# Optimization experiments

Hardware: AMD Instinct MI355X
Metric: run time of the kernel (lower is better)

Reference implementation:

```python
import jax, jax.numpy as jnp
import numpy as np

N = 100000      # total sampled nodes
NT = 20000      # target (destination) nodes
E = 2000000     # edges
IN = 128        # in_dim
OUT = 64        # out_channels (heads=1, concat)
NEG_SLOPE = 0.2 # GATConv default negative_slope


def setup_inputs() -> dict:
    key = jax.random.key(0)
    ks = jax.random.split(key, 6)
    x = jax.random.normal(ks[0], (N, IN), dtype=jnp.float32)
    edge_src = jax.random.randint(ks[1], (E,), 0, N)
    edge_dst = jax.random.randint(ks[2], (E,), 0, NT)
    # GATConv params: shared lin for src/dst (in_channels is int), att vectors, bias
    W = jax.random.normal(ks[3], (IN, OUT), dtype=jnp.float32) / np.sqrt(IN).astype(np.float32)
    att_src = jax.random.normal(ks[4], (OUT,), dtype=jnp.float32)
    att_dst = jax.random.normal(ks[5], (OUT,), dtype=jnp.float32)
    bias = jnp.zeros((OUT,), dtype=jnp.float32)
    return {"x": x, "edge_src": edge_src, "edge_dst": edge_dst,
            "W": W, "att_src": att_src, "att_dst": att_dst, "bias": bias,
            "num_target": NT}


def reference(x, edge_src, edge_dst, W, att_src, att_dst, bias, num_target):
    # Linear transform (lin_src == lin_dst in PyG GATConv when in_channels is int)
    x_proj = x @ W                      # [N, OUT]
    x_dst = x_proj[:num_target]         # [NT, OUT] target nodes are x[:num_target]
    # Per-node attention logits
    a_src = x_proj @ att_src            # [N]
    a_dst = x_dst @ att_dst             # [NT]
    # Edge logits + LeakyReLU
    e = jax.nn.leaky_relu(a_src[edge_src] + a_dst[edge_dst], NEG_SLOPE)  # [E]
    # Segment softmax over edges grouped by destination
    m = jax.ops.segment_max(e, edge_dst, num_segments=num_target)
    m = jnp.where(jnp.isneginf(m), jnp.float32(0.0), m)  # empty segments
    p = jnp.exp(e - m[edge_dst])
    denom = jax.ops.segment_sum(p, edge_dst, num_segments=num_target)
    alpha = p / (denom[edge_dst] + jnp.float32(1e-16))   # PyG softmax eps
    # Weighted scatter-aggregate of source features
    out = jax.ops.segment_sum(alpha[:, None] * x_proj[edge_src], edge_dst,
                              num_segments=num_target)   # [NT, OUT]
    return out + bias
```

## Files before the change

kernel.cpp:

```cpp
#include <hip/hip_runtime.h>

#define IN_DIM 128
#define OUT_DIM 64
#define NEG_SLOPE 0.2f

#define NBUCK 625
#define BCAP 4096
#define CHUNK 8192

typedef __attribute__((ext_vector_type(8))) short short8v;
typedef __attribute__((ext_vector_type(4))) float f32x4;

__device__ __forceinline__ unsigned pack_bf16(float a, float b) {
    unsigned ua = __float_as_uint(a), ub = __float_as_uint(b);
    ua += 0x7FFFu + ((ua >> 16) & 1u);
    ub += 0x7FFFu + ((ub >> 16) & 1u);
    return (ua >> 16) | (ub & 0xFFFF0000u);
}

__device__ __forceinline__ short8v mk8(unsigned a, unsigned b, unsigned c, unsigned d) {
    union { uint4 u; short8v s; } z;
    z.u = make_uint4(a, b, c, d);
    return z.s;
}

__global__ __launch_bounds__(1024) void part_kernel(
    const float* __restrict__ W, unsigned* __restrict__ w_hi,
    unsigned* __restrict__ w_lo,
    const int* __restrict__ edge_src, const int* __restrict__ edge_dst,
    int* __restrict__ bcursor, unsigned* __restrict__ inter, int E)
{
    if (blockIdx.x == 0) {
        int g = threadIdx.x;
        int kb = g >> 6, col = g & 63;
        unsigned uh[4], ul[4];
#pragma unroll
        for (int i = 0; i < 4; ++i) {
            float a = W[(kb * 8 + 2 * i) * 64 + col];
            float b = W[(kb * 8 + 2 * i + 1) * 64 + col];
            unsigned h = pack_bf16(a, b);
            float la = a - __uint_as_float(h << 16);
            float lb = b - __uint_as_float(h & 0xFFFF0000u);
            uh[i] = h;
            ul[i] = pack_bf16(la, lb);
        }
        *(uint4*)(w_hi + g * 4) = make_uint4(uh[0], uh[1], uh[2], uh[3]);
        *(uint4*)(w_lo + g * 4) = make_uint4(ul[0], ul[1], ul[2], ul[3]);
        return;
    }

    __shared__ unsigned stage[CHUNK];
    __shared__ int hist[NBUCK];
    __shared__ int loff[NBUCK];
    __shared__ int gbase[NBUCK];
    __shared__ int cur[NBUCK];
    __shared__ int wsum[16];

    const int t  = threadIdx.x;
    const int c0 = (blockIdx.x - 1) * CHUNK;
    const int cnt = min(CHUNK, E - c0);

    for (int i = t; i < NBUCK; i += 1024) hist[i] = 0;
    __syncthreads();

    unsigned pk[8];
    int nmine = 0;
    const int i0 = 8 * t;
    if (i0 + 8 <= cnt) {
        int4 s0 = *(const int4*)(edge_src + c0 + i0);
        int4 s1 = *(const int4*)(edge_src + c0 + i0 + 4);
        int4 d0 = *(const int4*)(edge_dst + c0 + i0);
        int4 d1 = *(const int4*)(edge_dst + c0 + i0 + 4);
        pk[0] = ((unsigned)d0.x << 17) | (unsigned)s0.x;
        pk[1] = ((unsigned)d0.y << 17) | (unsigned)s0.y;
        pk[2] = ((unsigned)d0.z << 17) | (unsigned)s0.z;
        pk[3] = ((unsigned)d0.w << 17) | (unsigned)s0.w;
        pk[4] = ((unsigned)d1.x << 17) | (unsigned)s1.x;
        pk[5] = ((unsigned)d1.y << 17) | (unsigned)s1.y;
        pk[6] = ((unsigned)d1.z << 17) | (unsigned)s1.z;
        pk[7] = ((unsigned)d1.w << 17) | (unsigned)s1.w;
        nmine = 8;
    } else {
#pragma unroll
        for (int k = 0; k < 8; ++k) {
            int i = i0 + k;
            if (i < cnt) {
                pk[k] = ((unsigned)edge_dst[c0 + i] << 17) | (unsigned)edge_src[c0 + i];
                nmine = k + 1;
            }
        }
    }
#pragma unroll
    for (int k = 0; k < 8; ++k)
        if (k < nmine) atomicAdd(&hist[pk[k] >> 22], 1);
    __syncthreads();

    {
        const int lane = t & 63, w = t >> 6;
        int v = (t < NBUCK) ? hist[t] : 0;
        int scan = v;
#pragma unroll
        for (int off = 1; off < 64; off <<= 1) {
            int o = __shfl_up(scan, off);
            if (lane >= off) scan += o;
        }
        if (lane == 63) wsum[w] = scan;
        __syncthreads();
        int wpre = 0;
#pragma unroll
        for (int i = 0; i < 16; ++i)
            if (i < w) wpre += wsum[i];
        int excl = wpre + scan - v;
        if (t < NBUCK) {
            loff[t] = excl;
            cur[t]  = excl;
            if (v > 0) gbase[t] = t * BCAP + atomicAdd(&bcursor[t], v);
        }
    }
    __syncthreads();

#pragma unroll
    for (int k = 0; k < 8; ++k)
        if (k < nmine) {
            unsigned v = pk[k];
            int p = atomicAdd(&cur[v >> 22], 1);
            stage[p] = v;
        }
    __syncthreads();

    for (int i = t; i < cnt; i += 1024) {
        unsigned v = stage[i];
        int b = v >> 22;
        int pos = gbase[b] + (i - loff[b]);
        if (pos < (b + 1) * BCAP) inter[pos] = v;
    }
}

__global__ __launch_bounds__(256) void gemm_kernel(
    const float* __restrict__ x,
    const unsigned* __restrict__ w_hi, const unsigned* __restrict__ w_lo,
    const float* __restrict__ att_src, const float* __restrict__ att_dst,
    unsigned* __restrict__ x_bf, float* __restrict__ a_src,
    float* __restrict__ a_dst, int N, int NT)
{
    __shared__ __align__(16) float C[128 * 64];

    const int t    = threadIdx.x;
    const int lane = t & 63;
    const int w    = t >> 6;
    const int r0   = blockIdx.x * 128;
    const int rsub = lane & 15;
    const int kg   = lane >> 4;

    const int r1 = min(r0 + 32 * w + rsub,      N - 1);
    const int r2 = min(r0 + 32 * w + 16 + rsub, N - 1);
    const float* xrow1 = x + (size_t)r1 * IN_DIM + kg * 8;
    const float* xrow2 = x + (size_t)r2 * IN_DIM + kg * 8;

    float4 xv[16];
#pragma unroll
    for (int j = 0; j < 8; ++j)
        xv[j] = *(const float4*)(xrow1 + (j >> 1) * 32 + (j & 1) * 4);
#pragma unroll
    for (int j = 0; j < 8; ++j)
        xv[8 + j] = *(const float4*)(xrow2 + (j >> 1) * 32 + (j & 1) * 4);
    __builtin_amdgcn_sched_barrier(0);

    short8v ah[2][4], al[2][4];
#pragma unroll
    for (int rf = 0; rf < 2; ++rf)
#pragma unroll
        for (int ks = 0; ks < 4; ++ks) {
            float4 v0 = xv[8 * rf + 2 * ks], v1 = xv[8 * rf + 2 * ks + 1];
            unsigned h0 = pack_bf16(v0.x, v0.y);
            unsigned h1 = pack_bf16(v0.z, v0.w);
            unsigned h2 = pack_bf16(v1.x, v1.y);
            unsigned h3 = pack_bf16(v1.z, v1.w);
            unsigned l0 = pack_bf16(v0.x - __uint_as_float(h0 << 16),
                                    v0.y - __uint_as_float(h0 & 0xFFFF0000u));
            unsigned l1 = pack_bf16(v0.z - __uint_as_float(h1 << 16),
                                    v0.w - __uint_as_float(h1 & 0xFFFF0000u));
            unsigned l2 = pack_bf16(v1.x - __uint_as_float(h2 << 16),
                                    v1.y - __uint_as_float(h2 & 0xFFFF0000u));
            unsigned l3 = pack_bf16(v1.z - __uint_as_float(h3 << 16),
                                    v1.w - __uint_as_float(h3 & 0xFFFF0000u));
            ah[rf][ks] = mk8(h0, h1, h2, h3);
            al[rf][ks] = mk8(l0, l1, l2, l3);
        }

    f32x4 acc[2][4];
#pragma unroll
    for (int rf = 0; rf < 2; ++rf)
#pragma unroll
        for (int cf = 0; cf < 4; ++cf) acc[rf][cf] = f32x4{0.f, 0.f, 0.f, 0.f};

#pragma unroll
    for (int ks = 0; ks < 4; ++ks) {
        const int kb = 4 * ks + kg;
        const unsigned* bhp = w_hi + (kb * 64 + rsub) * 4;
        const unsigned* blp = w_lo + (kb * 64 + rsub) * 4;
        short8v bh[4], bl[4];
#pragma unroll
        for (int cf = 0; cf < 4; ++cf) {
            bh[cf] = *(const short8v*)(bhp + cf * 64);
            bl[cf] = *(const short8v*)(blp + cf * 64);
        }
#pragma unroll
        for (int cf = 0; cf < 4; ++cf) {
#pragma unroll
            for (int rf = 0; rf < 2; ++rf) {
                acc[rf][cf] = __builtin_amdgcn_mfma_f32_16x16x32_bf16(ah[rf][ks], bh[cf], acc[rf][cf], 0, 0, 0);
                acc[rf][cf] = __builtin_amdgcn_mfma_f32_16x16x32_bf16(al[rf][ks], bh[cf], acc[rf][cf], 0, 0, 0);
                acc[rf][cf] = __builtin_amdgcn_mfma_f32_16x16x32_bf16(ah[rf][ks], bl[cf], acc[rf][cf], 0, 0, 0);
            }
        }
    }

#pragma unroll
    for (int rf = 0; rf < 2; ++rf)
#pragma unroll
        for (int cf = 0; cf < 4; ++cf)
#pragma unroll
            for (int j = 0; j < 4; ++j) {
                int row = 32 * w + 16 * rf + 4 * kg + j;
                int col = 16 * cf + rsub;
                C[row * 64 + ((col + 4 * row) & 63)] = acc[rf][cf][j];
            }
    __syncthreads();

    {
        const int row = t >> 1;
        const int h   = t & 1;
        const int rr  = r0 + row;
        float v[32];
#pragma unroll
        for (int j = 0; j < 8; ++j) {
            int s = (32 * h + 4 * j + 4 * row) & 63;
            float4 f = *(const float4*)(C + row * 64 + s);
            v[4 * j + 0] = f.x; v[4 * j + 1] = f.y;
            v[4 * j + 2] = f.z; v[4 * j + 3] = f.w;
        }
        if (rr < N) {
            unsigned pk[16];
#pragma unroll
            for (int m = 0; m < 16; ++m)
                pk[m] = pack_bf16(v[2 * m], v[2 * m + 1]);
            unsigned* dst = x_bf + (size_t)rr * 32 + h * 16;
            *(uint4*)(dst + 0)  = make_uint4(pk[0], pk[1], pk[2], pk[3]);
            *(uint4*)(dst + 4)  = make_uint4(pk[4], pk[5], pk[6], pk[7]);
            *(uint4*)(dst + 8)  = make_uint4(pk[8], pk[9], pk[10], pk[11]);
            *(uint4*)(dst + 12) = make_uint4(pk[12], pk[13], pk[14], pk[15]);

            float ps = 0.f, pd = 0.f;
#pragma unroll
            for (int i = 0; i < 32; ++i) {
                ps = fmaf(v[i], att_src[32 * h + i], ps);
                pd = fmaf(v[i], att_dst[32 * h + i], pd);
            }
            ps += __shfl_xor(ps, 1);
            pd += __shfl_xor(pd, 1);
            if (h == 0) {
                a_src[rr] = ps;
                if (rr < NT) a_dst[rr] = pd;
            }
        }
    }
}

#define LRELU_EXP(a) __expf(((a) > 0.f ? (a) : NEG_SLOPE * (a)))

__global__ __launch_bounds__(512) void agg_kernel(
    const int* __restrict__ bcursor, const unsigned* __restrict__ inter,
    const float* __restrict__ a_src, const float* __restrict__ a_dst,
    const unsigned* __restrict__ x_bf, const float* __restrict__ bias,
    float* __restrict__ out, int NT)
{
    __shared__ unsigned ssrc[BCAP];
    __shared__ int cnt[32], off_[32], cur[32];

    const int b = blockIdx.x;
    const int t = threadIdx.x;
    const int base = b * BCAP;
    const int n = min(bcursor[b], BCAP);

    if (t < 32) cnt[t] = 0;
    __syncthreads();

    unsigned ev[8];
#pragma unroll
    for (int k = 0; k < 8; ++k) {
        int i = t + 512 * k;
        ev[k] = 0xFFFFFFFFu;
        if (i < n) {
            ev[k] = inter[base + i];
            atomicAdd(&cnt[(ev[k] >> 17) & 31], 1);
        }
    }
    __syncthreads();

    if (t == 0) {
        int r = 0;
#pragma unroll
        for (int j = 0; j < 32; ++j) { off_[j] = r; r += cnt[j]; }
    }
    __syncthreads();
    if (t < 32) cur[t] = off_[t];
    __syncthreads();

#pragma unroll
    for (int k = 0; k < 8; ++k)
        if (ev[k] != 0xFFFFFFFFu) {
            int p = atomicAdd(&cur[(ev[k] >> 17) & 31], 1);
            ssrc[p] = ev[k] & 0x1FFFFu;
        }
    __syncthreads();

    const int lane = t & 63;
    const int w    = t >> 6;
    const int g    = lane >> 3;
    const int sub  = lane & 7;

    float4 b0 = *(const float4*)(bias + sub * 8);
    float4 b1 = *(const float4*)(bias + sub * 8 + 4);

    for (int q = 0; q < 4; ++q) {
        const int ld  = w + 8 * q;
        const int tgt = b * 32 + ld;
        if (tgt >= NT) continue;

        const int lo = off_[ld];
        const int nn = cnt[ld];
        const int hi = lo + nn;

        if (nn <= 0) {
            if (g == 0) {
                float* o = out + (size_t)tgt * OUT_DIM + sub * 8;
                *(float4*)(o)     = b0;
                *(float4*)(o + 4) = b1;
            }
            continue;
        }

        const float ad = a_dst[tgt];
        const int nc = (nn + 63) >> 6;

        float dl = 0.f;
        float acc[8];
#pragma unroll
        for (int k = 0; k < 8; ++k) acc[k] = 0.f;

        int c = 0;
        for (; c + 1 < nc; c += 2) {
            const int iA = lo + 64 * c + lane;
            const int iB = iA + 64;
            const int sA = (int)ssrc[iA];
            const int sB = (iB < hi) ? (int)ssrc[iB] : 0;

            int s8A[8], s8B[8];
#pragma unroll
            for (int j = 0; j < 8; ++j) s8A[j] = __shfl(sA, 8 * g + j);
#pragma unroll
            for (int j = 0; j < 8; ++j) s8B[j] = __shfl(sB, 8 * g + j);

            uint4 vA[8], vB[8];
#pragma unroll
            for (int j = 0; j < 8; ++j)
                vA[j] = *(const uint4*)(x_bf + (size_t)s8A[j] * 32 + sub * 4);
#pragma unroll
            for (int j = 0; j < 8; ++j)
                vB[j] = *(const uint4*)(x_bf + (size_t)s8B[j] * 32 + sub * 4);

            const float aA = a_src[sA];
            const float aB = a_src[sB];
            const float pA = LRELU_EXP(aA + ad);
            const float pB = (iB < hi) ? LRELU_EXP(aB + ad) : 0.f;
            dl += pA + pB;

            float p8A[8], p8B[8];
#pragma unroll
            for (int j = 0; j < 8; ++j) p8A[j] = __shfl(pA, 8 * g + j);
#pragma unroll
            for (int j = 0; j < 8; ++j) p8B[j] = __shfl(pB, 8 * g + j);

#pragma unroll
            for (int j = 0; j < 8; ++j) {
                const float p = p8A[j];
                acc[0] = fmaf(p, __uint_as_float(vA[j].x << 16), acc[0]);
                acc[1] = fmaf(p, __uint_as_float(vA[j].x & 0xFFFF0000u), acc[1]);
                acc[2] = fmaf(p, __uint_as_float(vA[j].y << 16), acc[2]);
                acc[3] = fmaf(p, __uint_as_float(vA[j].y & 0xFFFF0000u), acc[3]);
                acc[4] = fmaf(p, __uint_as_float(vA[j].z << 16), acc[4]);
                acc[5] = fmaf(p, __uint_as_float(vA[j].z & 0xFFFF0000u), acc[5]);
                acc[6] = fmaf(p, __uint_as_float(vA[j].w << 16), acc[6]);
                acc[7] = fmaf(p, __uint_as_float(vA[j].w & 0xFFFF0000u), acc[7]);
            }
#pragma unroll
            for (int j = 0; j < 8; ++j) {
                const float p = p8B[j];
                acc[0] = fmaf(p, __uint_as_float(vB[j].x << 16), acc[0]);
                acc[1] = fmaf(p, __uint_as_float(vB[j].x & 0xFFFF0000u), acc[1]);
                acc[2] = fmaf(p, __uint_as_float(vB[j].y << 16), acc[2]);
                acc[3] = fmaf(p, __uint_as_float(vB[j].y & 0xFFFF0000u), acc[3]);
                acc[4] = fmaf(p, __uint_as_float(vB[j].z << 16), acc[4]);
                acc[5] = fmaf(p, __uint_as_float(vB[j].z & 0xFFFF0000u), acc[5]);
                acc[6] = fmaf(p, __uint_as_float(vB[j].w << 16), acc[6]);
                acc[7] = fmaf(p, __uint_as_float(vB[j].w & 0xFFFF0000u), acc[7]);
            }
        }
        if (c < nc) {
            const int iA = lo + 64 * c + lane;
            const int sA = (iA < hi) ? (int)ssrc[iA] : 0;
            int s8A[8];
#pragma unroll
            for (int j = 0; j < 8; ++j) s8A[j] = __shfl(sA, 8 * g + j);
            uint4 vA[8];
#pragma unroll
            for (int j = 0; j < 8; ++j)
                vA[j] = *(const uint4*)(x_bf + (size_t)s8A[j] * 32 + sub * 4);
            const float aA = a_src[sA];
            const float pA = (iA < hi) ? LRELU_EXP(aA + ad) : 0.f;
            dl += pA;
            float p8A[8];
#pragma unroll
            for (int j = 0; j < 8; ++j) p8A[j] = __shfl(pA, 8 * g + j);
#pragma unroll
            for (int j = 0; j < 8; ++j) {
                const float p = p8A[j];
                acc[0] = fmaf(p, __uint_as_float(vA[j].x << 16), acc[0]);
                acc[1] = fmaf(p, __uint_as_float(vA[j].x & 0xFFFF0000u), acc[1]);
                acc[2] = fmaf(p, __uint_as_float(vA[j].y << 16), acc[2]);
                acc[3] = fmaf(p, __uint_as_float(vA[j].y & 0xFFFF0000u), acc[3]);
                acc[4] = fmaf(p, __uint_as_float(vA[j].z << 16), acc[4]);
                acc[5] = fmaf(p, __uint_as_float(vA[j].z & 0xFFFF0000u), acc[5]);
                acc[6] = fmaf(p, __uint_as_float(vA[j].w << 16), acc[6]);
                acc[7] = fmaf(p, __uint_as_float(vA[j].w & 0xFFFF0000u), acc[7]);
            }
        }

#pragma unroll
        for (int k = 0; k < 8; ++k) {
            acc[k] += __shfl_xor(acc[k], 8);
            acc[k] += __shfl_xor(acc[k], 16);
            acc[k] += __shfl_xor(acc[k], 32);
        }
#pragma unroll
        for (int off = 32; off; off >>= 1) dl += __shfl_xor(dl, off);
        const float inv = 1.f / (dl + 1e-16f);

        if (g == 0) {
            float* o = out + (size_t)tgt * OUT_DIM + sub * 8;
            float4 o0, o1;
            o0.x = fmaf(acc[0], inv, b0.x); o0.y = fmaf(acc[1], inv, b0.y);
            o0.z = fmaf(acc[2], inv, b0.z); o0.w = fmaf(acc[3], inv, b0.w);
            o1.x = fmaf(acc[4], inv, b1.x); o1.y = fmaf(acc[5], inv, b1.y);
            o1.z = fmaf(acc[6], inv, b1.z); o1.w = fmaf(acc[7], inv, b1.w);
            *(float4*)(o)     = o0;
            *(float4*)(o + 4) = o1;
        }
    }
}

extern "C" void kernel_launch(void* const* d_in, const int* in_sizes, int n_in,
                              void* d_out, int out_size, void* d_ws, size_t ws_size,
                              hipStream_t stream)
{
    const float* x        = (const float*)d_in[0];
    const int*   edge_src = (const int*)d_in[1];
    const int*   edge_dst = (const int*)d_in[2];
    const float* W        = (const float*)d_in[3];
    const float* att_src  = (const float*)d_in[4];
    const float* att_dst  = (const float*)d_in[5];
    const float* bias     = (const float*)d_in[6];

    const int N  = in_sizes[0] / IN_DIM;
    const int E  = in_sizes[1];
    const int NT = out_size / OUT_DIM;
    float* out = (float*)d_out;

    auto align256 = [](size_t v) { return (v + 255) & ~(size_t)255; };
    char* w = (char*)d_ws;
    unsigned* x_bf   = (unsigned*)w;  w += align256((size_t)N * 32 * 4);
    float*    a_src  = (float*)w;     w += align256((size_t)N * 4);
    float*    a_dst  = (float*)w;     w += align256((size_t)NT * 4);
    int*      bcursor= (int*)w;       w += align256((size_t)NBUCK * 4);
    unsigned* w_hi   = (unsigned*)w;  w += align256((size_t)1024 * 16);
    unsigned* w_lo   = (unsigned*)w;  w += align256((size_t)1024 * 16);
    unsigned* inter  = (unsigned*)w;  w += align256((size_t)NBUCK * BCAP * 4);

    hipMemsetAsync(bcursor, 0, (size_t)NBUCK * 4, stream);

    const int nchunk = (E + CHUNK - 1) / CHUNK;
    part_kernel<<<1 + nchunk, 1024, 0, stream>>>(
        W, w_hi, w_lo, edge_src, edge_dst, bcursor, inter, E);

    gemm_kernel<<<(N + 127) / 128, 256, 0, stream>>>(
        x, w_hi, w_lo, att_src, att_dst, x_bf, a_src, a_dst, N, NT);

    agg_kernel<<<NBUCK, 512, 0, stream>>>(
        bcursor, inter, a_src, a_dst, x_bf, bias, out, NT);
}
```

Before: 93.72 us.

## Split each destination bucket into four source-range slices with partial-sum combine

Edges are partitioned by destination bucket and also by one of four source-index slices, which gives 2500 aggregation blocks instead of 625. Each block's gathers then touch a narrower range of x_bf, which should help cache locality, and the work is spread over more blocks. Each block writes partial numerators and denominators, and a new combine kernel sums the four slices, normalizes and adds bias. The cost is extra global traffic for the partials (4×NT×64 floats), one more kernel launch, and a finer scatter in the partition pass. The per-slice capacity cap of 1024 could drop edges if a slice overflows.

Result: slower. 100.1 us (+6.8%).

```diff
diff --git a/kernel.cpp b/kernel.cpp
--- a/kernel.cpp
+++ b/kernel.cpp
@@ -5,7 +5,8 @@
 #define NEG_SLOPE 0.2f
 
 #define NBUCK 625
-#define BCAP 4096
+#define NKEY  2500
+#define SCAP  1024
 #define CHUNK 8192
 
 typedef __attribute__((ext_vector_type(8))) short short8v;
@@ -24,11 +25,17 @@
     return z.s;
 }
 
+__device__ __forceinline__ int slice_of(unsigned src, float inv_sdiv) {
+    int s = (int)((float)src * inv_sdiv);
+    return s > 3 ? 3 : s;
+}
+
 __global__ __launch_bounds__(1024) void part_kernel(
     const float* __restrict__ W, unsigned* __restrict__ w_hi,
     unsigned* __restrict__ w_lo,
     const int* __restrict__ edge_src, const int* __restrict__ edge_dst,
-    int* __restrict__ bcursor, unsigned* __restrict__ inter, int E)
+    int* __restrict__ kcursor, unsigned* __restrict__ inter, int E,
+    float inv_sdiv)
 {
     if (blockIdx.x == 0) {
         int g = threadIdx.x;
@@ -50,20 +57,20 @@
     }
 
     __shared__ unsigned stage[CHUNK];
-    __shared__ int hist[NBUCK];
-    __shared__ int loff[NBUCK];
-    __shared__ int gbase[NBUCK];
-    __shared__ int cur[NBUCK];
+    __shared__ int hist[NKEY];
+    __shared__ int cur[NKEY];
+    __shared__ int delta[NKEY];
     __shared__ int wsum[16];
 
     const int t  = threadIdx.x;
     const int c0 = (blockIdx.x - 1) * CHUNK;
     const int cnt = min(CHUNK, E - c0);
 
-    for (int i = t; i < NBUCK; i += 1024) hist[i] = 0;
+    for (int i = t; i < NKEY; i += 1024) hist[i] = 0;
     __syncthreads();
 
     unsigned pk[8];
+    int ky[8];
     int nmine = 0;
     const int i0 = 8 * t;
     if (i0 + 8 <= cnt) {
@@ -92,13 +99,25 @@
     }
 #pragma unroll
     for (int k = 0; k < 8; ++k)
-        if (k < nmine) atomicAdd(&hist[pk[k] >> 22], 1);
+        if (k < nmine) {
+            ky[k] = (int)(pk[k] >> 22) * 4 + slice_of(pk[k] & 0x1FFFFu, inv_sdiv);
+            atomicAdd(&hist[ky[k]], 1);
+        }
     __syncthreads();
 
     {
+        int tmp[3], vv[3];
+        int mysum = 0;
+#pragma unroll
+        for (int k = 0; k < 3; ++k) {
+            int idx = t * 3 + k;
+            int v = (idx < NKEY) ? hist[idx] : 0;
+            vv[k] = v;
+            tmp[k] = mysum;
+            mysum += v;
+        }
         const int lane = t & 63, w = t >> 6;
-        int v = (t < NBUCK) ? hist[t] : 0;
-        int scan = v;
+        int scan = mysum;
 #pragma unroll
         for (int off = 1; off < 64; off <<= 1) {
             int o = __shfl_up(scan, off);
@@ -110,11 +129,18 @@
 #pragma unroll
         for (int i = 0; i < 16; ++i)
             if (i < w) wpre += wsum[i];
-        int excl = wpre + scan - v;
-        if (t < NBUCK) {
-            loff[t] = excl;
-            cur[t]  = excl;
-            if (v > 0) gbase[t] = t * BCAP + atomicAdd(&bcursor[t], v);
+        int excl = wpre + scan - mysum;
+#pragma unroll
+        for (int k = 0; k < 3; ++k) {
+            int idx = t * 3 + k;
+            if (idx < NKEY) {
+                int e = excl + tmp[k];
+                cur[idx] = e;
+                if (vv[k] > 0) {
+                    int gb = atomicAdd(&kcursor[idx], vv[k]);
+                    delta[idx] = gb - e;
+                }
+            }
         }
     }
     __syncthreads();
@@ -122,17 +148,16 @@
 #pragma unroll
     for (int k = 0; k < 8; ++k)
         if (k < nmine) {
-            unsigned v = pk[k];
-            int p = atomicAdd(&cur[v >> 22], 1);
-            stage[p] = v;
+            int p = atomicAdd(&cur[ky[k]], 1);
+            stage[p] = pk[k];
         }
     __syncthreads();
 
     for (int i = t; i < cnt; i += 1024) {
         unsigned v = stage[i];
-        int b = v >> 22;
-        int pos = gbase[b] + (i - loff[b]);
-        if (pos < (b + 1) * BCAP) inter[pos] = v;
+        int kk = (int)(v >> 22) * 4 + slice_of(v & 0x1FFFFu, inv_sdiv);
+        int off = delta[kk] + i;
+        if ((unsigned)off < SCAP) inter[kk * SCAP + off] = v;
     }
 }
 
@@ -270,25 +295,27 @@
 #define LRELU_EXP(a) __expf(((a) > 0.f ? (a) : NEG_SLOPE * (a)))
 
 __global__ __launch_bounds__(512) void agg_kernel(
-    const int* __restrict__ bcursor, const unsigned* __restrict__ inter,
+    const int* __restrict__ kcursor, const unsigned* __restrict__ inter,
     const float* __restrict__ a_src, const float* __restrict__ a_dst,
-    const unsigned* __restrict__ x_bf, const float* __restrict__ bias,
-    float* __restrict__ out, int NT)
+    const unsigned* __restrict__ x_bf,
+    float* __restrict__ num4, float* __restrict__ den4, int NT)
 {
-    __shared__ unsigned ssrc[BCAP];
+    __shared__ unsigned ssrc[SCAP];
     __shared__ int cnt[32], off_[32], cur[32];
 
-    const int b = blockIdx.x;
-    const int t = threadIdx.x;
-    const int base = b * BCAP;
-    const int n = min(bcursor[b], BCAP);
+    const int key  = blockIdx.x;
+    const int b    = key >> 2;
+    const int s    = key & 3;
+    const int t    = threadIdx.x;
+    const int base = key * SCAP;
+    const int n    = min(kcursor[key], SCAP);
 
     if (t < 32) cnt[t] = 0;
     __syncthreads();
 
-    unsigned ev[8];
-#pragma unroll
-    for (int k = 0; k < 8; ++k) {
+    unsigned ev[2];
+#pragma unroll
+    for (int k = 0; k < 2; ++k) {
         int i = t + 512 * k;
         ev[k] = 0xFFFFFFFFu;
         if (i < n) {
@@ -308,7 +335,7 @@
     __syncthreads();
 
 #pragma unroll
-    for (int k = 0; k < 8; ++k)
+    for (int k = 0; k < 2; ++k)
         if (ev[k] != 0xFFFFFFFFu) {
             int p = atomicAdd(&cur[(ev[k] >> 17) & 31], 1);
             ssrc[p] = ev[k] & 0x1FFFFu;
@@ -317,147 +344,99 @@
 
     const int lane = t & 63;
     const int w    = t >> 6;
-    const int g    = lane >> 3;
+    const int q    = lane >> 4;
+    const int g    = (lane >> 3) & 1;
     const int sub  = lane & 7;
 
-    float4 b0 = *(const float4*)(bias + sub * 8);
-    float4 b1 = *(const float4*)(bias + sub * 8 + 4);
-
-    for (int q = 0; q < 4; ++q) {
-        const int ld  = w + 8 * q;
-        const int tgt = b * 32 + ld;
-        if (tgt >= NT) continue;
-
-        const int lo = off_[ld];
-        const int nn = cnt[ld];
-        const int hi = lo + nn;
-
-        if (nn <= 0) {
-            if (g == 0) {
-                float* o = out + (size_t)tgt * OUT_DIM + sub * 8;
-                *(float4*)(o)     = b0;
-                *(float4*)(o + 4) = b1;
-            }
-            continue;
-        }
-
-        const float ad = a_dst[tgt];
-        const int nc = (nn + 63) >> 6;
-
-        float dl = 0.f;
-        float acc[8];
-#pragma unroll
-        for (int k = 0; k < 8; ++k) acc[k] = 0.f;
-
-        int c = 0;
-        for (; c + 1 < nc; c += 2) {
-            const int iA = lo + 64 * c + lane;
-            const int iB = iA + 64;
-            const int sA = (int)ssrc[iA];
-            const int sB = (iB < hi) ? (int)ssrc[iB] : 0;
-
-            int s8A[8], s8B[8];
-#pragma unroll
-            for (int j = 0; j < 8; ++j) s8A[j] = __shfl(sA, 8 * g + j);
-#pragma unroll
-            for (int j = 0; j < 8; ++j) s8B[j] = __shfl(sB, 8 * g + j);
-
-            uint4 vA[8], vB[8];
-#pragma unroll
-            for (int j = 0; j < 8; ++j)
-                vA[j] = *(const uint4*)(x_bf + (size_t)s8A[j] * 32 + sub * 4);
-#pragma unroll
-            for (int j = 0; j < 8; ++j)
-                vB[j] = *(const uint4*)(x_bf + (size_t)s8B[j] * 32 + sub * 4);
-
-            const float aA = a_src[sA];
-            const float aB = a_src[sB];
-            const float pA = LRELU_EXP(aA + ad);
-            const float pB = (iB < hi) ? LRELU_EXP(aB + ad) : 0.f;
-            dl += pA + pB;
-
-            float p8A[8], p8B[8];
-#pragma unroll
-            for (int j = 0; j < 8; ++j) p8A[j] = __shfl(pA, 8 * g + j);
-#pragma unroll
-            for (int j = 0; j < 8; ++j) p8B[j] = __shfl(pB, 8 * g + j);
-
-#pragma unroll
-            for (int j = 0; j < 8; ++j) {
-                const float p = p8A[j];
-                acc[0] = fmaf(p, __uint_as_float(vA[j].x << 16), acc[0]);
-                acc[1] = fmaf(p, __uint_as_float(vA[j].x & 0xFFFF0000u), acc[1]);
-                acc[2] = fmaf(p, __uint_as_float(vA[j].y << 16), acc[2]);
-                acc[3] = fmaf(p, __uint_as_float(vA[j].y & 0xFFFF0000u), acc[3]);
-                acc[4] = fmaf(p, __uint_as_float(vA[j].z << 16), acc[4]);
-                acc[5] = fmaf(p, __uint_as_float(vA[j].z & 0xFFFF0000u), acc[5]);
-                acc[6] = fmaf(p, __uint_as_float(vA[j].w << 16), acc[6]);
-                acc[7] = fmaf(p, __uint_as_float(vA[j].w & 0xFFFF0000u), acc[7]);
-            }
-#pragma unroll
-            for (int j = 0; j < 8; ++j) {
-                const float p = p8B[j];
-                acc[0] = fmaf(p, __uint_as_float(vB[j].x << 16), acc[0]);
-                acc[1] = fmaf(p, __uint_as_float(vB[j].x & 0xFFFF0000u), acc[1]);
-                acc[2] = fmaf(p, __uint_as_float(vB[j].y << 16), acc[2]);
-                acc[3] = fmaf(p, __uint_as_float(vB[j].y & 0xFFFF0000u), acc[3]);
-                acc[4] = fmaf(p, __uint_as_float(vB[j].z << 16), acc[4]);
-                acc[5] = fmaf(p, __uint_as_float(vB[j].z & 0xFFFF0000u), acc[5]);
-                acc[6] = fmaf(p, __uint_as_float(vB[j].w << 16), acc[6]);
-                acc[7] = fmaf(p, __uint_as_float(vB[j].w & 0xFFFF0000u), acc[7]);
-            }
-        }
-        if (c < nc) {
-            const int iA = lo + 64 * c + lane;
-            const int sA = (iA < hi) ? (int)ssrc[iA] : 0;
-            int s8A[8];
-#pragma unroll
-            for (int j = 0; j < 8; ++j) s8A[j] = __shfl(sA, 8 * g + j);
-            uint4 vA[8];
-#pragma unroll
-            for (int j = 0; j < 8; ++j)
-                vA[j] = *(const uint4*)(x_bf + (size_t)s8A[j] * 32 + sub * 4);
-            const float aA = a_src[sA];
-            const float pA = (iA < hi) ? LRELU_EXP(aA + ad) : 0.f;
-            dl += pA;
-            float p8A[8];
-#pragma unroll
-            for (int j = 0; j < 8; ++j) p8A[j] = __shfl(pA, 8 * g + j);
-#pragma unroll
-            for (int j = 0; j < 8; ++j) {
-                const float p = p8A[j];
-                acc[0] = fmaf(p, __uint_as_float(vA[j].x << 16), acc[0]);
-                acc[1] = fmaf(p, __uint_as_float(vA[j].x & 0xFFFF0000u), acc[1]);
-                acc[2] = fmaf(p, __uint_as_float(vA[j].y << 16), acc[2]);
-                acc[3] = fmaf(p, __uint_as_float(vA[j].y & 0xFFFF0000u), acc[3]);
-                acc[4] = fmaf(p, __uint_as_float(vA[j].z << 16), acc[4]);
-                acc[5] = fmaf(p, __uint_as_float(vA[j].z & 0xFFFF0000u), acc[5]);
-                acc[6] = fmaf(p, __uint_as_float(vA[j].w << 16), acc[6]);
-                acc[7] = fmaf(p, __uint_as_float(vA[j].w & 0xFFFF0000u), acc[7]);
-            }
-        }
-
-#pragma unroll
-        for (int k = 0; k < 8; ++k) {
-            acc[k] += __shfl_xor(acc[k], 8);
-            acc[k] += __shfl_xor(acc[k], 16);
-            acc[k] += __shfl_xor(acc[k], 32);
-        }
-#pragma unroll
-        for (int off = 32; off; off >>= 1) dl += __shfl_xor(dl, off);
-        const float inv = 1.f / (dl + 1e-16f);
-
-        if (g == 0) {
-            float* o = out + (size_t)tgt * OUT_DIM + sub * 8;
-            float4 o0, o1;
-            o0.x = fmaf(acc[0], inv, b0.x); o0.y = fmaf(acc[1], inv, b0.y);
-            o0.z = fmaf(acc[2], inv, b0.z); o0.w = fmaf(acc[3], inv, b0.w);
-            o1.x = fmaf(acc[4], inv, b1.x); o1.y = fmaf(acc[5], inv, b1.y);
-            o1.z = fmaf(acc[6], inv, b1.z); o1.w = fmaf(acc[7], inv, b1.w);
-            *(float4*)(o)     = o0;
-            *(float4*)(o + 4) = o1;
-        }
-    }
+    const int ld  = 4 * w + q;
+    const int tgt = b * 32 + ld;
+
+    const int lo = off_[ld];
+    const int nn = cnt[ld];
+
+    int myc = (nn + 15) >> 4;
+    int ncmax = myc;
+    ncmax = max(ncmax, __shfl_xor(ncmax, 16));
+    ncmax = max(ncmax, __shfl_xor(ncmax, 32));
+
+    const float ad = (tgt < NT) ? a_dst[tgt] : 0.f;
+
+    float dl = 0.f;
+    float acc[8];
+#pragma unroll
+    for (int k = 0; k < 8; ++k) acc[k] = 0.f;
+
+    for (int c = 0; c < ncmax; ++c) {
+        const int el = 16 * c + 8 * g + sub;
+        const bool valid = el < nn;
+        const int sA = valid ? (int)ssrc[lo + el] : 0;
+
+        int s8[8];
+#pragma unroll
+        for (int j = 0; j < 8; ++j) s8[j] = __shfl(sA, 16 * q + 8 * g + j);
+
+        uint4 v[8];
+#pragma unroll
+        for (int j = 0; j < 8; ++j)
+            v[j] = *(const uint4*)(x_bf + (size_t)s8[j] * 32 + sub * 4);
+
+        const float aA = a_src[sA];
+        const float pA = valid ? LRELU_EXP(aA + ad) : 0.f;
+        dl += pA;
+
+        float p8[8];
+#pragma unroll
+        for (int j = 0; j < 8; ++j) p8[j] = __shfl(pA, 16 * q + 8 * g + j);
+
+#pragma unroll
+        for (int j = 0; j < 8; ++j) {
+            const float p = p8[j];
+            acc[0] = fmaf(p, __uint_as_float(v[j].x << 16), acc[0]);
+            acc[1] = fmaf(p, __uint_as_float(v[j].x & 0xFFFF0000u), acc[1]);
+            acc[2] = fmaf(p, __uint_as_float(v[j].y << 16), acc[2]);
+            acc[3] = fmaf(p, __uint_as_float(v[j].y & 0xFFFF0000u), acc[3]);
+            acc[4] = fmaf(p, __uint_as_float(v[j].z << 16), acc[4]);
+            acc[5] = fmaf(p, __uint_as_float(v[j].z & 0xFFFF0000u), acc[5]);
+            acc[6] = fmaf(p, __uint_as_float(v[j].w << 16), acc[6]);
+            acc[7] = fmaf(p, __uint_as_float(v[j].w & 0xFFFF0000u), acc[7]);
+        }
+    }
+
+#pragma unroll
+    for (int k = 0; k < 8; ++k) acc[k] += __shfl_xor(acc[k], 8);
+    dl += __shfl_xor(dl, 1);
+    dl += __shfl_xor(dl, 2);
+    dl += __shfl_xor(dl, 4);
+    dl += __shfl_xor(dl, 8);
+
+    if (g == 0 && tgt < NT) {
+        float* np = num4 + ((size_t)s * NT + tgt) * OUT_DIM + sub * 8;
+        float4 o0, o1;
+        o0.x = acc[0]; o0.y = acc[1]; o0.z = acc[2]; o0.w = acc[3];
+        o1.x = acc[4]; o1.y = acc[5]; o1.z = acc[6]; o1.w = acc[7];
+        *(float4*)(np)     = o0;
+        *(float4*)(np + 4) = o1;
+        if (sub == 0) den4[s * NT + tgt] = dl;
+    }
+}
+
+__global__ __launch_bounds__(256) void combine_kernel(
+    const float* __restrict__ num4, const float* __restrict__ den4,
+    const float* __restrict__ bias, float* __restrict__ out, int NT)
+{
+    const int t   = threadIdx.x;
+    const int tgt = blockIdx.x * 4 + (t >> 6);
+    const int col = t & 63;
+    if (tgt >= NT) return;
+
+    float d = 1e-16f;
+    float v = 0.f;
+#pragma unroll
+    for (int s = 0; s < 4; ++s) {
+        d += den4[s * NT + tgt];
+        v += num4[((size_t)s * NT + tgt) * OUT_DIM + col];
+    }
+    out[(size_t)tgt * OUT_DIM + col] = fmaf(v, 1.f / d, bias[col]);
 }
 
 extern "C" void kernel_launch(void* const* d_in, const int* in_sizes, int n_in,
@@ -477,25 +456,33 @@
     const int NT = out_size / OUT_DIM;
     float* out = (float*)d_out;
 
+    const int sdiv = (N + 3) / 4;
+    const float inv_sdiv = 1.0f / (float)sdiv;
+
     auto align256 = [](size_t v) { return (v + 255) & ~(size_t)255; };
     char* w = (char*)d_ws;
     unsigned* x_bf   = (unsigned*)w;  w += align256((size_t)N * 32 * 4);
     float*    a_src  = (float*)w;     w += align256((size_t)N * 4);
     float*    a_dst  = (float*)w;     w += align256((size_t)NT * 4);
-    int*      bcursor= (int*)w;       w += align256((size_t)NBUCK * 4);
+    int*      kcursor= (int*)w;       w += align256((size_t)NKEY * 4);
     unsigned* w_hi   = (unsigned*)w;  w += align256((size_t)1024 * 16);
     unsigned* w_lo   = (unsigned*)w;  w += align256((size_t)1024 * 16);
-    unsigned* inter  = (unsigned*)w;  w += align256((size_t)NBUCK * BCAP * 4);
-
-    hipMemsetAsync(bcursor, 0, (size_t)NBUCK * 4, stream);
+    float*    num4   = (float*)w;     w += align256((size_t)4 * NT * OUT_DIM * 4);
+    float*    den4   = (float*)w;     w += align256((size_t)4 * NT * 4);
+    unsigned* inter  = (unsigned*)w;  w += align256((size_t)NKEY * SCAP * 4);
+
+    hipMemsetAsync(kcursor, 0, (size_t)NKEY * 4, stream);
 
     const int nchunk = (E + CHUNK - 1) / CHUNK;
     part_kernel<<<1 + nchunk, 1024, 0, stream>>>(
-        W, w_hi, w_lo, edge_src, edge_dst, bcursor, inter, E);
+        W, w_hi, w_lo, edge_src, edge_dst, kcursor, inter, E, inv_sdiv);
 
     gemm_kernel<<<(N + 127) / 128, 256, 0, stream>>>(
         x, w_hi, w_lo, att_src, att_dst, x_bf, a_src, a_dst, N, NT);
 
-    agg_kernel<<<NBUCK, 512, 0, stream>>>(
-        bcursor, inter, a_src, a_dst, x_bf, bias, out, NT);
-}
+    agg_kernel<<<NKEY, 512, 0, stream>>>(
+        kcursor, inter, a_src, a_dst, x_bf, num4, den4, NT);
+
+    combine_kernel<<<(NT + 3) / 4, 256, 0, stream>>>(
+        num4, den4, bias, out, NT);
+}
```
